# Kernel tuning notes

Hardware: AMD Instinct MI355X
Metric: run time of the kernel (lower is better)

Reference implementation:

```python
import jax, jax.numpy as jnp
import numpy as np

T = 524288
AABB = 4.0
BETA_MIN = 0.1
L_ENC = 4
NL = np.array([16, 22, 30, 42, 58, 80, 111, 154, 213, 295, 407, 563, 777, 1074, 1483, 2048])
# corner offsets, same ordering as the torch code's vertices[:,0..7]
OFFS = np.array([[0,0,0],[1,0,0],[0,1,0],[1,1,0],[0,0,1],[1,0,1],[0,1,1],[1,1,1]])
PRIMES = np.array([1, 2654435761, 805459861], dtype=np.uint32)


def hash_features(xn, tables):
    # xn: [N,3] normalized positions in hash-grid space; tables: [16, T, 2]
    Ns = jnp.asarray(NL, jnp.float32)                      # [16]
    xs = xn[:, None, :] * Ns[None, :, None]                # [N,16,3]
    fl = jnp.floor(xs)
    loc = xs - fl                                          # trilinear weights input
    fli = fl.astype(jnp.int32).astype(jnp.uint32)          # wraparound == int32 bit pattern
    offs = jnp.asarray(OFFS, jnp.uint32)                   # [8,3]
    pr = jnp.asarray(PRIMES, jnp.uint32)
    # spatial hash per corner, per level (avoid materializing [N,16,8,3] vertices)
    a = (fli[:, :, None, 0] + offs[None, None, :, 0]) * pr[0]
    b = (fli[:, :, None, 1] + offs[None, None, :, 1]) * pr[1]
    c = (fli[:, :, None, 2] + offs[None, None, :, 2]) * pr[2]
    h = ((a ^ b) ^ c) % jnp.uint32(T)                      # [N,16,8]
    lvl_off = (jnp.arange(len(NL), dtype=jnp.uint32) * jnp.uint32(T))[None, :, None]
    flat_idx = (h + lvl_off).astype(jnp.int32)             # index into flattened tables
    feats = tables.reshape(-1, tables.shape[-1])[flat_idx] # [N,16,8,2] gather
    offf = jnp.asarray(OFFS, jnp.float32)
    lp = loc[:, :, None, :]
    w = jnp.prod(lp * offf + (1.0 - lp) * (1.0 - offf), axis=-1)  # [N,16,8]
    out = jnp.einsum('nlc,nlcf->nlf', w, feats)            # trilinear interp
    return out.reshape(out.shape[0], -1)                   # [N, 16*2], level-major


def pos_enc(d):
    parts = [d]
    for j in range(L_ENC):
        parts.append(jnp.sin((2.0 ** j) * d))
        parts.append(jnp.cos((2.0 ** j) * d))
    return jnp.concatenate(parts, axis=1)                  # [N,27]


def _forward(x, d, appearance_idx, transient_idx, tables, emb_a, emb_t,
             Wd1, bd1, Wd2, bd2, Ws1, bs1, Ws2, bs2, Ws3, bs3,
             Wt1, bt1, Wt2, bt2, Wt3, bt3, Wtd, btd, Wtr, btr, Wtb, btb):
    xn = x / AABB
    mask = (jnp.abs(xn[:, 0]) < 0.5) & (jnp.abs(xn[:, 1]) < 0.5) & (jnp.abs(xn[:, 2]) < 0.5)
    xn = xn + 0.5
    feats = hash_features(xn, tables)                      # [N,32]
    h = jnp.maximum(feats @ Wd1 + bd1, 0.0) @ Wd2 + bd2    # density MLP -> [N,16]
    denc = pos_enc(d)
    a_emb = emb_a[appearance_idx]
    t_emb = emb_t[transient_idx]
    s = jnp.concatenate([h, denc, a_emb], axis=1)
    s = jnp.maximum(s @ Ws1 + bs1, 0.0)
    s = jnp.maximum(s @ Ws2 + bs2, 0.0)
    srgb = jax.nn.sigmoid(s @ Ws3 + bs3)
    t = jnp.concatenate([h, t_emb], axis=1)
    t = jnp.maximum(t @ Wt1 + bt1, 0.0)
    t = jnp.maximum(t @ Wt2 + bt2, 0.0)
    t = jnp.maximum(t @ Wt3 + bt3, 0.0)
    tsig = jax.nn.softplus(t @ Wtd + btd)[:, 0]
    trgb = jax.nn.sigmoid(t @ Wtr + btr)
    tbeta = jax.nn.softplus(t @ Wtb + btb)[:, 0] + BETA_MIN
    m = mask[:, None]
    static_rgb = jnp.where(m, srgb, 0.0)
    static_sigma = jnp.exp(jnp.where(mask, h[:, 0], -100000.0))
    transient_rgb = jnp.where(m, trgb, 0.0)
    transient_sigma = jnp.exp(jnp.where(mask, tsig, -100000.0))
    transient_beta = jnp.where(mask, tbeta, BETA_MIN)
    return static_rgb, static_sigma, transient_rgb, transient_sigma, transient_beta


def setup_inputs() -> dict:
    key = jax.random.key(0)
    ks = jax.random.split(key, 24)
    N, NV = 262144, 1000

    def lin(k, i, o):
        return jax.random.normal(k, (i, o), jnp.float32) * (1.0 / np.sqrt(i))

    inp = {}
    inp['x'] = jax.random.normal(ks[0], (N, 3), jnp.float32)
    inp['d'] = jax.random.normal(ks[1], (N, 3), jnp.float32)
    inp['appearance_idx'] = jax.random.randint(ks[2], (N,), 0, NV)
    inp['transient_idx'] = jax.random.randint(ks[3], (N,), 0, NV)
    inp['tables'] = (jax.random.uniform(ks[4], (len(NL), T, 2), jnp.float32) * 2 - 1) * 1e-4
    inp['emb_a'] = jax.random.normal(ks[5], (NV, 48), jnp.float32)
    inp['emb_t'] = jax.random.normal(ks[6], (NV, 16), jnp.float32)
    inp['Wd1'] = lin(ks[7], 32, 64); inp['bd1'] = jnp.zeros((64,), jnp.float32)
    inp['Wd2'] = lin(ks[8], 64, 16); inp['bd2'] = jnp.zeros((16,), jnp.float32)
    inp['Ws1'] = lin(ks[9], 91, 64); inp['bs1'] = jnp.zeros((64,), jnp.float32)
    inp['Ws2'] = lin(ks[10], 64, 64); inp['bs2'] = jnp.zeros((64,), jnp.float32)
    inp['Ws3'] = lin(ks[11], 64, 3); inp['bs3'] = jnp.zeros((3,), jnp.float32)
    inp['Wt1'] = lin(ks[12], 32, 64); inp['bt1'] = jnp.zeros((64,), jnp.float32)
    inp['Wt2'] = lin(ks[13], 64, 64); inp['bt2'] = jnp.zeros((64,), jnp.float32)
    inp['Wt3'] = lin(ks[14], 64, 64); inp['bt3'] = jnp.zeros((64,), jnp.float32)
    inp['Wtd'] = lin(ks[15], 64, 1); inp['btd'] = jnp.zeros((1,), jnp.float32)
    inp['Wtr'] = lin(ks[16], 64, 3); inp['btr'] = jnp.zeros((3,), jnp.float32)
    inp['Wtb'] = lin(ks[17], 64, 1); inp['btb'] = jnp.zeros((1,), jnp.float32)
    return inp


def reference(x, d, appearance_idx, transient_idx, tables, emb_a, emb_t,
              Wd1, bd1, Wd2, bd2, Ws1, bs1, Ws2, bs2, Ws3, bs3,
              Wt1, bt1, Wt2, bt2, Wt3, bt3, Wtd, btd, Wtr, btr, Wtb, btb):
    return _forward(x, d, appearance_idx, transient_idx, tables, emb_a, emb_t,
                    Wd1, bd1, Wd2, bd2, Ws1, bs1, Ws2, bs2, Ws3, bs3,
                    Wt1, bt1, Wt2, bt2, Wt3, bt3, Wtd, btd, Wtr, btr, Wtb, btb)
```

## Files before the change

kernel.cpp:

```cpp
#include <hip/hip_runtime.h>
#include <hip/hip_fp16.h>
#include <math.h>

#define NT 256
#define NT0 512
#define T_SIZE 524288u
#define T_MASK 524287u
#define PR1 2654435761u
#define PR2 805459861u

#define OFF_WD1 0
#define OFF_WD2 4096
#define OFF_WS1 6144
#define OFF_WS2 18432
#define OFF_WT1 26624
#define OFF_WT2 30720
#define OFF_WT3 38912
#define WBUF_USH 47104
#define WBUF_BYTES 98304

typedef float f32x4 __attribute__((ext_vector_type(4)));
typedef short s16x8 __attribute__((ext_vector_type(8)));
typedef unsigned u32x4 __attribute__((ext_vector_type(4)));

__device__ __forceinline__ float sigmoidf_(float x) { return 1.0f / (1.0f + __expf(-x)); }
__device__ __forceinline__ float softplusf_(float x) { return fmaxf(x, 0.0f) + log1pf(__expf(-fabsf(x))); }

__device__ __forceinline__ unsigned short f2bf(float f) {
  union { float f; unsigned u; } v; v.f = f;
  unsigned r = v.u + 0x7fffu + ((v.u >> 16) & 1u);
  return (unsigned short)(r >> 16);
}
__device__ __forceinline__ float bf2f(unsigned short h) {
  union { unsigned u; float f; } v; v.u = ((unsigned)h) << 16; return v.f;
}
__device__ __forceinline__ f32x4 splat4(float t) { f32x4 v; v[0]=t; v[1]=t; v[2]=t; v[3]=t; return v; }

__device__ __forceinline__ unsigned char f2e5(float f) {
  unsigned short u = __half_as_ushort(__float2half(f));
  return (unsigned char)(((unsigned)u + 0x7Fu + ((u >> 8) & 1u)) >> 8);
}
__device__ __forceinline__ float e52f(unsigned v) {
  return __half2float(__ushort_as_half((unsigned short)((v & 0xFFu) << 8)));
}

template <int ASTR, int SWM>
__device__ __forceinline__ s16x8 lda(const unsigned short* act, int lane, int m, int kh) {
  int p = m * 16 + (lane & 15);
  int c = (kh * 32 + ((lane >> 4) << 3)) ^ ((p & SWM) << 3);
  return *reinterpret_cast<const s16x8*>(act + p * ASTR + c);
}
__device__ __forceinline__ s16x8 ldb(const unsigned short* wb, int lane, int fidx) {
  return *reinterpret_cast<const s16x8*>(wb + (fidx * 64 + lane) * 8);
}
template <int ASTR, int SWM>
__device__ __forceinline__ void stp(unsigned short* act, int p, int col, float v0, float v1) {
  unsigned pk = (unsigned)f2bf(v0) | (((unsigned)f2bf(v1)) << 16);
  *reinterpret_cast<unsigned*>(act + p * ASTR + (col ^ ((p & SWM) << 3))) = pk;
}

template <int BT, int KH, int NTI, int NCOLS, class F>
__device__ void stage_plane(unsigned short* dst, const float* __restrict__ W, int plane, int tid, F rowmap) {
  for (int i = tid; i < NTI * KH * 64; i += BT) {
    int f = i >> 6, lane = i & 63;
    int n = f / KH, kh = f - n * KH;
    int o = n * 16 + (lane & 15);
    int kb = kh * 32 + ((lane >> 4) << 3);
    unsigned us0, us1, us2, us3;
#define MKPAIR(dstu, j0) { \
      unsigned short e0, e1; \
      { int sr = rowmap(kb + (j0)); float w = (sr >= 0) ? W[sr * NCOLS + o] : 0.f; \
        unsigned short hi = f2bf(w); e0 = plane ? f2bf(w - bf2f(hi)) : hi; } \
      { int sr = rowmap(kb + (j0) + 1); float w = (sr >= 0) ? W[sr * NCOLS + o] : 0.f; \
        unsigned short hi = f2bf(w); e1 = plane ? f2bf(w - bf2f(hi)) : hi; } \
      dstu = (unsigned)e0 | (((unsigned)e1) << 16); }
    MKPAIR(us0, 0) MKPAIR(us1, 2) MKPAIR(us2, 4) MKPAIR(us3, 6)
#undef MKPAIR
    *reinterpret_cast<uint4*>(dst + (size_t)i * 8) = make_uint4(us0, us1, us2, us3);
  }
}

template <int BT>
__device__ __forceinline__ void stage(float* dst, const float* __restrict__ src, int cnt, int tid) {
  for (int i = tid; i < cnt; i += BT) dst[i] = src[i];
}

template <int BT>
__device__ __forceinline__ void stagecpy(unsigned short* dst, const unsigned short* __restrict__ src,
                                         int cnt_ush, int tid) {
  const uint4* s = reinterpret_cast<const uint4*>(src);
  uint4* d = reinterpret_cast<uint4*>(dst);
  for (int i = tid; i < (cnt_ush >> 3); i += BT) d[i] = s[i];
}

#define MFMA_(a, b, c) __builtin_amdgcn_mfma_f32_16x16x32_bf16(a, b, c, 0, 0, 0)

#define DECL_ACC f32x4 acc00, acc01, acc02, acc03, acc10, acc11, acc12, acc13, \
                       acc20, acc21, acc22, acc23, acc30, acc31, acc32, acc33;

#define ACC_INIT(B) { \
  float t0 = (B)[(lane & 15)], t1 = (B)[16 + (lane & 15)], t2 = (B)[32 + (lane & 15)], t3 = (B)[48 + (lane & 15)]; \
  acc00 = splat4(t0); acc10 = acc00; acc20 = acc00; acc30 = acc00; \
  acc01 = splat4(t1); acc11 = acc01; acc21 = acc01; acc31 = acc01; \
  acc02 = splat4(t2); acc12 = acc02; acc22 = acc02; acc32 = acc02; \
  acc03 = splat4(t3); acc13 = acc03; acc23 = acc03; acc33 = acc03; }

#define GEMM_NBLK(WPTR, kh, KH, n) { s16x8 b = ldb(WPTR, lane, (n) * (KH) + (kh)); \
  acc0##n = MFMA_(a0, b, acc0##n); acc1##n = MFMA_(a1, b, acc1##n); \
  acc2##n = MFMA_(a2, b, acc2##n); acc3##n = MFMA_(a3, b, acc3##n); }

#define GEMM64(ACTP, ASTR, SWM, WB, KH, PLN) { \
  _Pragma("unroll") for (int kh = 0; kh < (KH); ++kh) { \
    s16x8 a0 = lda<ASTR, SWM>(ACTP, lane, 0, kh), a1 = lda<ASTR, SWM>(ACTP, lane, 1, kh), \
          a2 = lda<ASTR, SWM>(ACTP, lane, 2, kh), a3 = lda<ASTR, SWM>(ACTP, lane, 3, kh); \
    _Pragma("unroll") for (int pl = 0; pl < (PLN); ++pl) { \
      const unsigned short* wp = (WB) + pl * (KH) * 2048; \
      GEMM_NBLK(wp, kh, KH, 0) GEMM_NBLK(wp, kh, KH, 1) GEMM_NBLK(wp, kh, KH, 2) GEMM_NBLK(wp, kh, KH, 3) } } }

#define ST_ACT1(ACTP, ASTR, SWM, m, n, A) { \
  _Pragma("unroll") for (int r = 0; r < 4; ++r) { \
    int p = (m) * 16 + ((lane >> 4) << 2) + r; int col = (n) * 16 + (lane & 15); \
    (ACTP)[p * (ASTR) + (col ^ ((p & (SWM)) << 3))] = f2bf(fmaxf((A)[r], 0.f)); } }

#define ST_ACT_ALL(ACTP, ASTR, SWM) \
  ST_ACT1(ACTP, ASTR, SWM, 0, 0, acc00) ST_ACT1(ACTP, ASTR, SWM, 0, 1, acc01) \
  ST_ACT1(ACTP, ASTR, SWM, 0, 2, acc02) ST_ACT1(ACTP, ASTR, SWM, 0, 3, acc03) \
  ST_ACT1(ACTP, ASTR, SWM, 1, 0, acc10) ST_ACT1(ACTP, ASTR, SWM, 1, 1, acc11) \
  ST_ACT1(ACTP, ASTR, SWM, 1, 2, acc12) ST_ACT1(ACTP, ASTR, SWM, 1, 3, acc13) \
  ST_ACT1(ACTP, ASTR, SWM, 2, 0, acc20) ST_ACT1(ACTP, ASTR, SWM, 2, 1, acc21) \
  ST_ACT1(ACTP, ASTR, SWM, 2, 2, acc22) ST_ACT1(ACTP, ASTR, SWM, 2, 3, acc23) \
  ST_ACT1(ACTP, ASTR, SWM, 3, 0, acc30) ST_ACT1(ACTP, ASTR, SWM, 3, 1, acc31) \
  ST_ACT1(ACTP, ASTR, SWM, 3, 2, acc32) ST_ACT1(ACTP, ASTR, SWM, 3, 3, acc33)

#define ST_HV(ACTP, ASTR, SWM, m, H) { \
  _Pragma("unroll") for (int r = 0; r < 4; ++r) { \
    int pp = (m) * 16 + ((lane >> 4) << 2) + r; \
    (ACTP)[pp * (ASTR) + ((lane & 15) ^ ((pp & (SWM)) << 3))] = f2bf((H)[r]); } }

__global__ void __launch_bounds__(256) kwprep(
    const float* __restrict__ Wd1, const float* __restrict__ Wd2,
    const float* __restrict__ Ws1, const float* __restrict__ Ws2,
    const float* __restrict__ Wt1, const float* __restrict__ Wt2,
    const float* __restrict__ Wt3, unsigned short* __restrict__ wbuf) {
  const int pid = blockIdx.x, tid = threadIdx.x;
  const float* W;
  int KH, NTI, NCOLS, mapt, dst;
  switch (pid >> 1) {
    case 0: W = Wd1; KH = 1; NTI = 4; NCOLS = 64; mapt = 0; dst = OFF_WD1 + (pid & 1) * 2048; break;
    case 1: W = Wd2; KH = 2; NTI = 1; NCOLS = 16; mapt = 0; dst = OFF_WD2 + (pid & 1) * 1024; break;
    case 2: W = Ws1; KH = 3; NTI = 4; NCOLS = 64; mapt = 1; dst = OFF_WS1 + (pid & 1) * 6144; break;
    case 3: W = Ws2; KH = 2; NTI = 4; NCOLS = 64; mapt = 0; dst = OFF_WS2 + (pid & 1) * 4096; break;
    case 4: W = Wt1; KH = 1; NTI = 4; NCOLS = 64; mapt = 0; dst = OFF_WT1 + (pid & 1) * 2048; break;
    case 5: W = Wt2; KH = 2; NTI = 4; NCOLS = 64; mapt = 0; dst = OFF_WT2 + (pid & 1) * 4096; break;
    default: W = Wt3; KH = 2; NTI = 4; NCOLS = 64; mapt = 0; dst = OFF_WT3 + (pid & 1) * 4096; break;
  }
  const int plane = pid & 1;
  const int total = NTI * KH * 64;
  for (int i = tid; i < total; i += 256) {
    int f = i >> 6, lane = i & 63;
    int n = f / KH, kh = f - n * KH;
    int o = n * 16 + (lane & 15);
    int kb = kh * 32 + ((lane >> 4) << 3);
    unsigned short e[8];
#pragma unroll
    for (int j = 0; j < 8; ++j) {
      int k = kb + j;
      int sr = mapt ? (k < 16 ? k : (k < 64 ? 27 + k : (k < 91 ? k - 48 : -1))) : k;
      float w = (sr >= 0) ? W[sr * NCOLS + o] : 0.f;
      unsigned short hi = f2bf(w);
      e[j] = plane ? f2bf(w - bf2f(hi)) : hi;
    }
    uint4 v;
    v.x = (unsigned)e[0] | ((unsigned)e[1] << 16);
    v.y = (unsigned)e[2] | ((unsigned)e[3] << 16);
    v.z = (unsigned)e[4] | ((unsigned)e[5] << 16);
    v.w = (unsigned)e[6] | ((unsigned)e[7] << 16);
    *reinterpret_cast<uint4*>(wbuf + dst + (size_t)i * 8) = v;
  }
}

__global__ void __launch_bounds__(256) kconv(const float* __restrict__ tables,
                                             unsigned* __restrict__ t8, int nq) {
  int i = blockIdx.x * 256 + threadIdx.x;
  if (i >= nq) return;
  f32x4 v = __builtin_nontemporal_load(reinterpret_cast<const f32x4*>(tables) + i);
  unsigned r = (unsigned)f2e5(v[0]) | ((unsigned)f2e5(v[1]) << 8) |
               ((unsigned)f2e5(v[2]) << 16) | ((unsigned)f2e5(v[3]) << 24);
  __builtin_nontemporal_store(r, t8 + i);
}

__global__ void __launch_bounds__(256, 4) k0a_gather(
    const float* __restrict__ x, const unsigned short* __restrict__ t8,
    unsigned* __restrict__ featws, int Npts) {
  const int lane = threadIdx.x & 63, wv = threadIdx.x >> 6;
  const int g = blockIdx.x & 3;
  const int n = (blockIdx.x >> 2) * 256 + wv * 64 + lane;
  if (n >= Npts) return;
  float xn0 = x[3 * n + 0] * 0.25f + 0.5f;
  float xn1 = x[3 * n + 1] * 0.25f + 0.5f;
  float xn2 = x[3 * n + 2] * 0.25f + 0.5f;

  float scA, scB, scC, scD;
  switch (g) {
    case 0:  scA = 16.f; scB = 58.f;  scC = 213.f; scD = 777.f;  break;
    case 1:  scA = 22.f; scB = 80.f;  scC = 295.f; scD = 1074.f; break;
    case 2:  scA = 30.f; scB = 111.f; scC = 407.f; scD = 1483.f; break;
    default: scA = 42.f; scB = 154.f; scC = 563.f; scD = 2048.f; break;
  }

#define ALVL(J, SC) \
  unsigned ad##J##0, ad##J##1, ad##J##2, ad##J##3, ad##J##4, ad##J##5, ad##J##6, ad##J##7; \
  float lf##J##0, lf##J##1, lf##J##2; \
  { \
    float xs0 = xn0 * (SC), xs1 = xn1 * (SC), xs2 = xn2 * (SC); \
    float f0 = floorf(xs0), f1 = floorf(xs1), f2 = floorf(xs2); \
    lf##J##0 = xs0 - f0; lf##J##1 = xs1 - f1; lf##J##2 = xs2 - f2; \
    unsigned i0 = (unsigned)(int)f0, i1 = (unsigned)(int)f1, i2 = (unsigned)(int)f2; \
    unsigned a0 = i0, a1 = i0 + 1u; \
    unsigned b0 = i1 * PR1, b1 = (i1 + 1u) * PR1; \
    unsigned c0 = i2 * PR2, c1 = (i2 + 1u) * PR2; \
    unsigned base = (unsigned)(g + 4 * (J)) * T_SIZE; \
    ad##J##0 = (base + ((a0 ^ b0 ^ c0) & T_MASK)) * 2u; \
    ad##J##1 = (base + ((a1 ^ b0 ^ c0) & T_MASK)) * 2u; \
    ad##J##2 = (base + ((a0 ^ b1 ^ c0) & T_MASK)) * 2u; \
    ad##J##3 = (base + ((a1 ^ b1 ^ c0) & T_MASK)) * 2u; \
    ad##J##4 = (base + ((a0 ^ b0 ^ c1) & T_MASK)) * 2u; \
    ad##J##5 = (base + ((a1 ^ b0 ^ c1) & T_MASK)) * 2u; \
    ad##J##6 = (base + ((a0 ^ b1 ^ c1) & T_MASK)) * 2u; \
    ad##J##7 = (base + ((a1 ^ b1 ^ c1) & T_MASK)) * 2u; \
  }
  ALVL(0, scA) ALVL(1, scB) ALVL(2, scC) ALVL(3, scD)
#undef ALVL

#define GLD(Q, AD) asm volatile("global_load_ushort %0, %1, %2" : "=v"(Q) : "v"(AD), "s"(t8));
#define LLVL(J) \
  unsigned q##J##0, q##J##1, q##J##2, q##J##3, q##J##4, q##J##5, q##J##6, q##J##7; \
  GLD(q##J##0, ad##J##0) GLD(q##J##1, ad##J##1) GLD(q##J##2, ad##J##2) GLD(q##J##3, ad##J##3) \
  GLD(q##J##4, ad##J##4) GLD(q##J##5, ad##J##5) GLD(q##J##6, ad##J##6) GLD(q##J##7, ad##J##7)
  LLVL(0) LLVL(1) LLVL(2) LLVL(3)
#undef LLVL
#undef GLD
  asm volatile("s_waitcnt vmcnt(0)" ::: "memory");
  __builtin_amdgcn_sched_barrier(0);

#define BLVL(J, FP) { \
    float w1x = lf##J##0, w0x = 1.f - w1x; \
    float w1y = lf##J##1, w0y = 1.f - w1y; \
    float w1z = lf##J##2, w0z = 1.f - w1z; \
    float w000 = w0x * w0y * w0z, w100 = w1x * w0y * w0z; \
    float w010 = w0x * w1y * w0z, w110 = w1x * w1y * w0z; \
    float w001 = w0x * w0y * w1z, w101 = w1x * w0y * w1z; \
    float w011 = w0x * w1y * w1z, w111 = w1x * w1y * w1z; \
    float fa = w000 * e52f(q##J##0) + w100 * e52f(q##J##1) + w010 * e52f(q##J##2) + \
               w110 * e52f(q##J##3) + w001 * e52f(q##J##4) + w101 * e52f(q##J##5) + \
               w011 * e52f(q##J##6) + w111 * e52f(q##J##7); \
    float fb = w000 * e52f(q##J##0 >> 8) + w100 * e52f(q##J##1 >> 8) + w010 * e52f(q##J##2 >> 8) + \
               w110 * e52f(q##J##3 >> 8) + w001 * e52f(q##J##4 >> 8) + w101 * e52f(q##J##5 >> 8) + \
               w011 * e52f(q##J##6 >> 8) + w111 * e52f(q##J##7 >> 8); \
    FP = (unsigned)f2bf(fa) | (((unsigned)f2bf(fb)) << 16); }
  unsigned fp0, fp1, fp2, fp3;
  BLVL(0, fp0) BLVL(1, fp1) BLVL(2, fp2) BLVL(3, fp3)
#undef BLVL
  u32x4 o; o[0] = fp0; o[1] = fp1; o[2] = fp2; o[3] = fp3;
  __builtin_nontemporal_store(
      o, reinterpret_cast<u32x4*>(featws + ((size_t)g * Npts + n) * 4));
}

__global__ void __launch_bounds__(NT, 2) k12b_all(
    const float* __restrict__ x, const float* __restrict__ d,
    const int* __restrict__ aidx, const int* __restrict__ tridx,
    const float* __restrict__ emb_a, const float* __restrict__ emb_t,
    const unsigned* __restrict__ featws, const unsigned short* __restrict__ wbuf,
    const float* __restrict__ bd1, const float* __restrict__ bd2,
    const float* __restrict__ bs1, const float* __restrict__ bs2,
    const float* __restrict__ Ws3, const float* __restrict__ bs3,
    const float* __restrict__ bt1, const float* __restrict__ bt2,
    const float* __restrict__ bt3,
    const float* __restrict__ Wtd, const float* __restrict__ btd,
    const float* __restrict__ Wtr, const float* __restrict__ btr,
    const float* __restrict__ Wtb, const float* __restrict__ btb,
    float* __restrict__ out, int Npts) {
  __shared__ __align__(16) unsigned short sh[36864];
  __shared__ __align__(16) float fl[1240];
  const int tid = threadIdx.x, lane = tid & 63, wv = tid >> 6;
  const int n = blockIdx.x * NT + tid;
  const bool live = (n < Npts);
  const int nn = live ? n : Npts - 1;
  unsigned short* actw = sh + wv * 6144;
  unsigned short* wreg = sh + 24576;
  const int p = lane;

  float xn0 = x[3 * nn + 0] * 0.25f, xn1 = x[3 * nn + 1] * 0.25f, xn2 = x[3 * nn + 2] * 0.25f;
  const bool mask = (fabsf(xn0) < 0.5f) && (fabsf(xn1) < 0.5f) && (fabsf(xn2) < 0.5f);

  u32x4 q0 = __builtin_nontemporal_load(
      reinterpret_cast<const u32x4*>(featws + ((size_t)0 * Npts + nn) * 4));
  u32x4 q1 = __builtin_nontemporal_load(
      reinterpret_cast<const u32x4*>(featws + ((size_t)1 * Npts + nn) * 4));
  u32x4 q2 = __builtin_nontemporal_load(
      reinterpret_cast<const u32x4*>(featws + ((size_t)2 * Npts + nn) * 4));
  u32x4 q3 = __builtin_nontemporal_load(
      reinterpret_cast<const u32x4*>(featws + ((size_t)3 * Npts + nn) * 4));
  const float4* tp = reinterpret_cast<const float4*>(emb_t + (size_t)tridx[nn] * 16);
  float4 et0 = tp[0], et1 = tp[1], et2 = tp[2], et3 = tp[3];

  {
    float d0 = d[3 * nn + 0], d1 = d[3 * nn + 1], d2 = d[3 * nn + 2];
    float s10 = __sinf(d0), s11 = __sinf(d1), s12 = __sinf(d2);
    float c10 = __cosf(d0), c11 = __cosf(d1), c12 = __cosf(d2);
    float s20 = __sinf(2.f * d0), s21 = __sinf(2.f * d1), s22 = __sinf(2.f * d2);
    float c20 = __cosf(2.f * d0), c21 = __cosf(2.f * d1), c22 = __cosf(2.f * d2);
    float s40 = __sinf(4.f * d0), s41 = __sinf(4.f * d1), s42 = __sinf(4.f * d2);
    float c40 = __cosf(4.f * d0), c41 = __cosf(4.f * d1), c42 = __cosf(4.f * d2);
    float s80 = __sinf(8.f * d0), s81 = __sinf(8.f * d1), s82 = __sinf(8.f * d2);
    float c80 = __cosf(8.f * d0), c81 = __cosf(8.f * d1), c82 = __cosf(8.f * d2);
    stp<96, 3>(actw, p, 64, d0, d1);   stp<96, 3>(actw, p, 66, d2, s10);
    stp<96, 3>(actw, p, 68, s11, s12); stp<96, 3>(actw, p, 70, c10, c11);
    stp<96, 3>(actw, p, 72, c12, s20); stp<96, 3>(actw, p, 74, s21, s22);
    stp<96, 3>(actw, p, 76, c20, c21); stp<96, 3>(actw, p, 78, c22, s40);
    stp<96, 3>(actw, p, 80, s41, s42); stp<96, 3>(actw, p, 82, c40, c41);
    stp<96, 3>(actw, p, 84, c42, s80); stp<96, 3>(actw, p, 86, s81, s82);
    stp<96, 3>(actw, p, 88, c80, c81); stp<96, 3>(actw, p, 90, c82, 0.f);
    stp<96, 3>(actw, p, 92, 0.f, 0.f); stp<96, 3>(actw, p, 94, 0.f, 0.f);
  }
#define PUTL96(l, val) *reinterpret_cast<unsigned*>(actw + p * 96 + ((2 * (l)) ^ ((p & 3) << 3))) = (val);
  PUTL96(0, q0[0]) PUTL96(4, q0[1]) PUTL96(8, q0[2]) PUTL96(12, q0[3])
  PUTL96(1, q1[0]) PUTL96(5, q1[1]) PUTL96(9, q1[2]) PUTL96(13, q1[3])
  PUTL96(2, q2[0]) PUTL96(6, q2[1]) PUTL96(10, q2[2]) PUTL96(14, q2[3])
  PUTL96(3, q3[0]) PUTL96(7, q3[1]) PUTL96(11, q3[2]) PUTL96(15, q3[3])
#undef PUTL96

  stagecpy<NT>(wreg, wbuf + OFF_WD1, 4096, tid);
  stagecpy<NT>(wreg + 4096, wbuf + OFF_WD2, 2048, tid);
  stage<NT>(fl, bs1, 64, tid);
  stage<NT>(fl + 64, bs2, 64, tid);
  stage<NT>(fl + 128, Ws3, 192, tid);
  if (tid < 3) fl[320 + tid] = bs3[tid];
  stage<NT>(fl + 384, bt1, 64, tid);
  stage<NT>(fl + 448, bt2, 64, tid);
  stage<NT>(fl + 512, bt3, 64, tid);
  stage<NT>(fl + 576, Wtd, 64, tid);
  stage<NT>(fl + 640, Wtr, 192, tid);
  stage<NT>(fl + 832, Wtb, 64, tid);
  if (tid == 0) { fl[896] = btd[0]; fl[900] = btb[0]; }
  if (tid < 3) fl[897 + tid] = btr[tid];
  stage<NT>(fl + 904, bd1, 64, tid);
  stage<NT>(fl + 968, bd2, 16, tid);
  __syncthreads();

  DECL_ACC;
  ACC_INIT(fl + 904);
  GEMM64(actw, 96, 3, wreg, 1, 2);
  ST_ACT_ALL(actw, 96, 3);

  f32x4 h0, h1, h2, h3;
  { float t = fl[968 + (lane & 15)]; h0 = splat4(t); h1 = h0; h2 = h0; h3 = h0; }
#pragma unroll
  for (int kh = 0; kh < 2; ++kh) {
    s16x8 a0 = lda<96, 3>(actw, lane, 0, kh), a1 = lda<96, 3>(actw, lane, 1, kh),
          a2 = lda<96, 3>(actw, lane, 2, kh), a3 = lda<96, 3>(actw, lane, 3, kh);
#pragma unroll
    for (int pl = 0; pl < 2; ++pl) {
      s16x8 b = ldb(wreg + 4096 + pl * 1024, lane, kh);
      h0 = MFMA_(a0, b, h0); h1 = MFMA_(a1, b, h1); h2 = MFMA_(a2, b, h2); h3 = MFMA_(a3, b, h3);
    }
  }
#define HV_X(m, H) { _Pragma("unroll") for (int r = 0; r < 4; ++r) { \
    int pr = (m) * 16 + ((lane >> 4) << 2) + r; \
    if ((lane & 15) == 0) fl[984 + wv * 64 + pr] = (H)[r]; } }
  HV_X(0, h0) HV_X(1, h1) HV_X(2, h2) HV_X(3, h3)
#undef HV_X
  ST_HV(actw, 96, 3, 0, h0) ST_HV(actw, 96, 3, 1, h1)
  ST_HV(actw, 96, 3, 2, h2) ST_HV(actw, 96, 3, 3, h3)
  {
    float hv0v = fl[984 + wv * 64 + lane];
    if (live) out[3 * (size_t)Npts + n] = mask ? __expf(hv0v) : 0.f;
  }
  {
    const float4* ap = reinterpret_cast<const float4*>(emb_a + (size_t)aidx[nn] * 48);
#pragma unroll
    for (int q = 0; q < 12; ++q) {
      float4 e = ap[q];
      stp<96, 3>(actw, p, 16 + 4 * q, e.x, e.y);
      stp<96, 3>(actw, p, 18 + 4 * q, e.z, e.w);
    }
  }
  __syncthreads();
  stagecpy<NT>(wreg, wbuf + OFF_WS1, 12288, tid);
  __syncthreads();

  ACC_INIT(fl);
  GEMM64(actw, 96, 3, wreg, 3, 2);
  ST_ACT_ALL(actw, 96, 3);
  __syncthreads();
  stagecpy<NT>(wreg, wbuf + OFF_WS2, 8192, tid);
  __syncthreads();
  ACC_INIT(fl + 64);
  GEMM64(actw, 96, 3, wreg, 2, 2);
  ST_ACT_ALL(actw, 96, 3);

  {
    float r0 = fl[320], r1 = fl[321], r2 = fl[322];
    for (int j = 0; j < 64; ++j) {
      float a = bf2f(actw[p * 96 + (j ^ ((p & 3) << 3))]);
      r0 = fmaf(a, fl[128 + 3 * j + 0], r0);
      r1 = fmaf(a, fl[128 + 3 * j + 1], r1);
      r2 = fmaf(a, fl[128 + 3 * j + 2], r2);
    }
    if (live) {
      out[3 * (size_t)n + 0] = mask ? sigmoidf_(r0) : 0.f;
      out[3 * (size_t)n + 1] = mask ? sigmoidf_(r1) : 0.f;
      out[3 * (size_t)n + 2] = mask ? sigmoidf_(r2) : 0.f;
    }
  }

  ST_HV(actw, 96, 3, 0, h0) ST_HV(actw, 96, 3, 1, h1)
  ST_HV(actw, 96, 3, 2, h2) ST_HV(actw, 96, 3, 3, h3)
  stp<96, 3>(actw, p, 16, et0.x, et0.y);  stp<96, 3>(actw, p, 18, et0.z, et0.w);
  stp<96, 3>(actw, p, 20, et1.x, et1.y);  stp<96, 3>(actw, p, 22, et1.z, et1.w);
  stp<96, 3>(actw, p, 24, et2.x, et2.y);  stp<96, 3>(actw, p, 26, et2.z, et2.w);
  stp<96, 3>(actw, p, 28, et3.x, et3.y);  stp<96, 3>(actw, p, 30, et3.z, et3.w);
  __syncthreads();
  stagecpy<NT>(wreg, wbuf + OFF_WT1, 4096, tid);
  __syncthreads();
  ACC_INIT(fl + 384);
  GEMM64(actw, 96, 3, wreg, 1, 2);
  ST_ACT_ALL(actw, 96, 3);
  __syncthreads();
  stagecpy<NT>(wreg, wbuf + OFF_WT2, 8192, tid);
  __syncthreads();
  ACC_INIT(fl + 448);
  GEMM64(actw, 96, 3, wreg, 2, 2);
  ST_ACT_ALL(actw, 96, 3);
  __syncthreads();
  stagecpy<NT>(wreg, wbuf + OFF_WT3, 8192, tid);
  __syncthreads();
  ACC_INIT(fl + 512);
  GEMM64(actw, 96, 3, wreg, 2, 2);
  ST_ACT_ALL(actw, 96, 3);

  float hd = fl[896], hr0 = fl[897], hr1 = fl[898], hr2 = fl[899], hb = fl[900];
  for (int j = 0; j < 64; ++j) {
    float a = bf2f(actw[p * 96 + (j ^ ((p & 3) << 3))]);
    hd = fmaf(a, fl[576 + j], hd);
    hr0 = fmaf(a, fl[640 + 3 * j + 0], hr0);
    hr1 = fmaf(a, fl[640 + 3 * j + 1], hr1);
    hr2 = fmaf(a, fl[640 + 3 * j + 2], hr2);
    hb = fmaf(a, fl[832 + j], hb);
  }
  if (live) {
    size_t N4 = (size_t)Npts * 4;
    out[N4 + 3 * (size_t)n + 0] = mask ? sigmoidf_(hr0) : 0.f;
    out[N4 + 3 * (size_t)n + 1] = mask ? sigmoidf_(hr1) : 0.f;
    out[N4 + 3 * (size_t)n + 2] = mask ? sigmoidf_(hr2) : 0.f;
    out[(size_t)Npts * 7 + n] = mask ? __expf(softplusf_(hd)) : 0.f;
    out[(size_t)Npts * 8 + n] = mask ? (softplusf_(hb) + 0.1f) : 0.1f;
  }
}

template <int F8>
__global__ void __launch_bounds__(NT0, 4) k0f_density(
    const float* __restrict__ x, const float* __restrict__ tables,
    const unsigned short* __restrict__ t8,
    const float* __restrict__ Wd1, const float* __restrict__ bd1,
    const float* __restrict__ Wd2, const float* __restrict__ bd2,
    float* __restrict__ hvws, float* __restrict__ out, int Npts) {
  __shared__ __align__(16) unsigned short sh[38912];
  __shared__ __align__(16) float fl[592];
  const int tid = threadIdx.x, lane = tid & 63, wv = tid >> 6;
  const int n = blockIdx.x * NT0 + tid;
  const bool live = (n < Npts);
  const int nn = live ? n : Npts - 1;

  stage_plane<NT0, 1, 4, 64>(sh + 32768, Wd1, 0, tid, [](int k) { return k; });
  stage_plane<NT0, 1, 4, 64>(sh + 32768 + 2048, Wd1, 1, tid, [](int k) { return k; });
  stage_plane<NT0, 2, 1, 16>(sh + 36864, Wd2, 0, tid, [](int k) { return k; });
  stage_plane<NT0, 2, 1, 16>(sh + 36864 + 1024, Wd2, 1, tid, [](int k) { return k; });
  stage<NT0>(fl, bd1, 64, tid);
  stage<NT0>(fl + 64, bd2, 16, tid);
  __syncthreads();

  unsigned short* actw = sh + wv * 4096;
  const int p = lane;
  float xn0 = x[3 * nn + 0] * 0.25f + 0.5f, xn1 = x[3 * nn + 1] * 0.25f + 0.5f, xn2 = x[3 * nn + 2] * 0.25f + 0.5f;
  const bool mask = (fabsf(xn0 - 0.5f) < 0.5f) && (fabsf(xn1 - 0.5f) < 0.5f) && (fabsf(xn2 - 0.5f) < 0.5f);

  const float2* tab2 = reinterpret_cast<const float2*>(tables);
  constexpr float NLV[16] = {16.f, 22.f, 30.f, 42.f, 58.f, 80.f, 111.f, 154.f,
                             213.f, 295.f, 407.f, 563.f, 777.f, 1074.f, 1483.f, 2048.f};
#pragma unroll
  for (int l = 0; l < 16; ++l) {
    const float sc = NLV[l];
    float xs0 = xn0 * sc, xs1 = xn1 * sc, xs2 = xn2 * sc;
    float f0 = floorf(xs0), f1 = floorf(xs1), f2 = floorf(xs2);
    float l0 = xs0 - f0, l1 = xs1 - f1, l2 = xs2 - f2;
    unsigned i0 = (unsigned)(int)f0, i1 = (unsigned)(int)f1, i2 = (unsigned)(int)f2;
    unsigned a0 = i0, a1 = i0 + 1u;
    unsigned b0 = i1 * PR1, b1 = (i1 + 1u) * PR1;
    unsigned c0 = i2 * PR2, c1 = (i2 + 1u) * PR2;
    float w0x = 1.f - l0, w1x = l0, w0y = 1.f - l1, w1y = l1, w0z = 1.f - l2, w1z = l2;
    float2 t0, t1, t2, t3, t4, t5, t6, t7;
    if constexpr (F8) {
      const unsigned short* tl8 = t8 + (size_t)l * T_SIZE;
      unsigned short q0 = tl8[(a0 ^ b0 ^ c0) & T_MASK];
      unsigned short q1 = tl8[(a1 ^ b0 ^ c0) & T_MASK];
      unsigned short q2 = tl8[(a0 ^ b1 ^ c0) & T_MASK];
      unsigned short q3 = tl8[(a1 ^ b1 ^ c0) & T_MASK];
      unsigned short q4 = tl8[(a0 ^ b0 ^ c1) & T_MASK];
      unsigned short q5 = tl8[(a1 ^ b0 ^ c1) & T_MASK];
      unsigned short q6 = tl8[(a0 ^ b1 ^ c1) & T_MASK];
      unsigned short q7 = tl8[(a1 ^ b1 ^ c1) & T_MASK];
      t0 = make_float2(e52f(q0), e52f(q0 >> 8));
      t1 = make_float2(e52f(q1), e52f(q1 >> 8));
      t2 = make_float2(e52f(q2), e52f(q2 >> 8));
      t3 = make_float2(e52f(q3), e52f(q3 >> 8));
      t4 = make_float2(e52f(q4), e52f(q4 >> 8));
      t5 = make_float2(e52f(q5), e52f(q5 >> 8));
      t6 = make_float2(e52f(q6), e52f(q6 >> 8));
      t7 = make_float2(e52f(q7), e52f(q7 >> 8));
    } else {
      const float2* tl = tab2 + (size_t)l * T_SIZE;
      t0 = tl[(a0 ^ b0 ^ c0) & T_MASK];
      t1 = tl[(a1 ^ b0 ^ c0) & T_MASK];
      t2 = tl[(a0 ^ b1 ^ c0) & T_MASK];
      t3 = tl[(a1 ^ b1 ^ c0) & T_MASK];
      t4 = tl[(a0 ^ b0 ^ c1) & T_MASK];
      t5 = tl[(a1 ^ b0 ^ c1) & T_MASK];
      t6 = tl[(a0 ^ b1 ^ c1) & T_MASK];
      t7 = tl[(a1 ^ b1 ^ c1) & T_MASK];
    }
    float w000 = w0x * w0y * w0z, w100 = w1x * w0y * w0z;
    float w010 = w0x * w1y * w0z, w110 = w1x * w1y * w0z;
    float w001 = w0x * w0y * w1z, w101 = w1x * w0y * w1z;
    float w011 = w0x * w1y * w1z, w111 = w1x * w1y * w1z;
    float fa = w000 * t0.x + w100 * t1.x + w010 * t2.x + w110 * t3.x +
               w001 * t4.x + w101 * t5.x + w011 * t6.x + w111 * t7.x;
    float fb = w000 * t0.y + w100 * t1.y + w010 * t2.y + w110 * t3.y +
               w001 * t4.y + w101 * t5.y + w011 * t6.y + w111 * t7.y;
    unsigned pk = (unsigned)f2bf(fa) | (((unsigned)f2bf(fb)) << 16);
    *reinterpret_cast<unsigned*>(actw + p * 64 + ((2 * l) ^ ((p & 7) << 3))) = pk;
  }

  DECL_ACC;
  ACC_INIT(fl);
  GEMM64(actw, 64, 7, sh + 32768, 1, 2);
  ST_ACT_ALL(actw, 64, 7);

  f32x4 h0, h1, h2, h3;
  { float t = fl[64 + (lane & 15)]; h0 = splat4(t); h1 = h0; h2 = h0; h3 = h0; }
  {
#pragma unroll
    for (int kh = 0; kh < 2; ++kh) {
      s16x8 a0 = lda<64, 7>(actw, lane, 0, kh), a1 = lda<64, 7>(actw, lane, 1, kh),
            a2 = lda<64, 7>(actw, lane, 2, kh), a3 = lda<64, 7>(actw, lane, 3, kh);
#pragma unroll
      for (int pl = 0; pl < 2; ++pl) {
        s16x8 b = ldb(sh + 36864 + pl * 1024, lane, kh);
        h0 = MFMA_(a0, b, h0); h1 = MFMA_(a1, b, h1); h2 = MFMA_(a2, b, h2); h3 = MFMA_(a3, b, h3);
      }
    }
  }
  const int ptbase = blockIdx.x * NT0 + wv * 64;
#define HV_ST(m, H) { _Pragma("unroll") for (int r = 0; r < 4; ++r) { \
    int pr = (m) * 16 + ((lane >> 4) << 2) + r; \
    if (ptbase + pr < Npts) hvws[(size_t)(ptbase + pr) * 16 + (lane & 15)] = (H)[r]; \
    if ((lane & 15) == 0) fl[80 + wv * 64 + pr] = (H)[r]; } }
  HV_ST(0, h0) HV_ST(1, h1) HV_ST(2, h2) HV_ST(3, h3)
#undef HV_ST
  float hv0 = fl[80 + wv * 64 + lane];
  if (live) out[3 * (size_t)Npts + n] = mask ? __expf(hv0) : 0.f;
}

__global__ void __launch_bounds__(NT, 2) k12_heads(
    const float* __restrict__ x, const float* __restrict__ d,
    const int* __restrict__ aidx, const int* __restrict__ tridx,
    const float* __restrict__ emb_a, const float* __restrict__ emb_t,
    const unsigned short* __restrict__ wbuf,
    const float* __restrict__ bs1, const float* __restrict__ bs2,
    const float* __restrict__ Ws3, const float* __restrict__ bs3,
    const float* __restrict__ bt1, const float* __restrict__ bt2,
    const float* __restrict__ bt3,
    const float* __restrict__ Wtd, const float* __restrict__ btd,
    const float* __restrict__ Wtr, const float* __restrict__ btr,
    const float* __restrict__ Wtb, const float* __restrict__ btb,
    const float* __restrict__ hvws, float* __restrict__ out, int Npts) {
  __shared__ __align__(16) unsigned short sh[36864];
  __shared__ __align__(16) float fl[904];
  const int tid = threadIdx.x, lane = tid & 63, wv = tid >> 6;
  const int n = blockIdx.x * NT + tid;
  const bool live = (n < Npts);
  const int nn = live ? n : Npts - 1;
  unsigned short* actw = sh + wv * 6144;
  const int p = lane;

  float xn0 = x[3 * nn + 0] * 0.25f, xn1 = x[3 * nn + 1] * 0.25f, xn2 = x[3 * nn + 2] * 0.25f;
  const bool mask = (fabsf(xn0) < 0.5f) && (fabsf(xn1) < 0.5f) && (fabsf(xn2) < 0.5f);

  const float4* hvp = reinterpret_cast<const float4*>(hvws + (size_t)nn * 16);
  float4 hv0_ = hvp[0], hv1_ = hvp[1], hv2_ = hvp[2], hv3_ = hvp[3];
  const float4* tp = reinterpret_cast<const float4*>(emb_t + (size_t)tridx[nn] * 16);
  float4 et0 = tp[0], et1 = tp[1], et2 = tp[2], et3 = tp[3];

  {
    stp<96, 3>(actw, p, 0, hv0_.x, hv0_.y);   stp<96, 3>(actw, p, 2, hv0_.z, hv0_.w);
    stp<96, 3>(actw, p, 4, hv1_.x, hv1_.y);   stp<96, 3>(actw, p, 6, hv1_.z, hv1_.w);
    stp<96, 3>(actw, p, 8, hv2_.x, hv2_.y);   stp<96, 3>(actw, p, 10, hv2_.z, hv2_.w);
    stp<96, 3>(actw, p, 12, hv3_.x, hv3_.y);  stp<96, 3>(actw, p, 14, hv3_.z, hv3_.w);
    const float4* ap = reinterpret_cast<const float4*>(emb_a + (size_t)aidx[nn] * 48);
#pragma unroll
    for (int q = 0; q < 12; ++q) {
      float4 e = ap[q];
      stp<96, 3>(actw, p, 16 + 4 * q, e.x, e.y);
      stp<96, 3>(actw, p, 18 + 4 * q, e.z, e.w);
    }
    float d0 = d[3 * nn + 0], d1 = d[3 * nn + 1], d2 = d[3 * nn + 2];
    float s10 = __sinf(d0), s11 = __sinf(d1), s12 = __sinf(d2);
    float c10 = __cosf(d0), c11 = __cosf(d1), c12 = __cosf(d2);
    float s20 = __sinf(2.f * d0), s21 = __sinf(2.f * d1), s22 = __sinf(2.f * d2);
    float c20 = __cosf(2.f * d0), c21 = __cosf(2.f * d1), c22 = __cosf(2.f * d2);
    float s40 = __sinf(4.f * d0), s41 = __sinf(4.f * d1), s42 = __sinf(4.f * d2);
    float c40 = __cosf(4.f * d0), c41 = __cosf(4.f * d1), c42 = __cosf(4.f * d2);
    float s80 = __sinf(8.f * d0), s81 = __sinf(8.f * d1), s82 = __sinf(8.f * d2);
    float c80 = __cosf(8.f * d0), c81 = __cosf(8.f * d1), c82 = __cosf(8.f * d2);
    stp<96, 3>(actw, p, 64, d0, d1);   stp<96, 3>(actw, p, 66, d2, s10);
    stp<96, 3>(actw, p, 68, s11, s12); stp<96, 3>(actw, p, 70, c10, c11);
    stp<96, 3>(actw, p, 72, c12, s20); stp<96, 3>(actw, p, 74, s21, s22);
    stp<96, 3>(actw, p, 76, c20, c21); stp<96, 3>(actw, p, 78, c22, s40);
    stp<96, 3>(actw, p, 80, s41, s42); stp<96, 3>(actw, p, 82, c40, c41);
    stp<96, 3>(actw, p, 84, c42, s80); stp<96, 3>(actw, p, 86, s81, s82);
    stp<96, 3>(actw, p, 88, c80, c81); stp<96, 3>(actw, p, 90, c82, 0.f);
    stp<96, 3>(actw, p, 92, 0.f, 0.f); stp<96, 3>(actw, p, 94, 0.f, 0.f);
  }
  stagecpy<NT>(sh + 24576, wbuf + OFF_WS1, 12288, tid);
  stage<NT>(fl, bs1, 64, tid);
  stage<NT>(fl + 64, bs2, 64, tid);
  stage<NT>(fl + 128, Ws3, 192, tid);
  if (tid < 3) fl[320 + tid] = bs3[tid];
  stage<NT>(fl + 384, bt1, 64, tid);
  stage<NT>(fl + 448, bt2, 64, tid);
  stage<NT>(fl + 512, bt3, 64, tid);
  stage<NT>(fl + 576, Wtd, 64, tid);
  stage<NT>(fl + 640, Wtr, 192, tid);
  stage<NT>(fl + 832, Wtb, 64, tid);
  if (tid == 0) { fl[896] = btd[0]; fl[900] = btb[0]; }
  if (tid < 3) fl[897 + tid] = btr[tid];
  __syncthreads();

  DECL_ACC;
  ACC_INIT(fl);
  GEMM64(actw, 96, 3, sh + 24576, 3, 2);
  ST_ACT_ALL(actw, 96, 3);
  __syncthreads();
  stagecpy<NT>(sh + 24576, wbuf + OFF_WS2, 8192, tid);
  __syncthreads();
  ACC_INIT(fl + 64);
  GEMM64(actw, 96, 3, sh + 24576, 2, 2);
  ST_ACT_ALL(actw, 96, 3);

  {
    float r0 = fl[320], r1 = fl[321], r2 = fl[322];
    for (int j = 0; j < 64; ++j) {
      float a = bf2f(actw[p * 96 + (j ^ ((p & 3) << 3))]);
      r0 = fmaf(a, fl[128 + 3 * j + 0], r0);
      r1 = fmaf(a, fl[128 + 3 * j + 1], r1);
      r2 = fmaf(a, fl[128 + 3 * j + 2], r2);
    }
    if (live) {
      out[3 * (size_t)n + 0] = mask ? sigmoidf_(r0) : 0.f;
      out[3 * (size_t)n + 1] = mask ? sigmoidf_(r1) : 0.f;
      out[3 * (size_t)n + 2] = mask ? sigmoidf_(r2) : 0.f;
    }
  }

  stp<96, 3>(actw, p, 0, hv0_.x, hv0_.y);   stp<96, 3>(actw, p, 2, hv0_.z, hv0_.w);
  stp<96, 3>(actw, p, 4, hv1_.x, hv1_.y);   stp<96, 3>(actw, p, 6, hv1_.z, hv1_.w);
  stp<96, 3>(actw, p, 8, hv2_.x, hv2_.y);   stp<96, 3>(actw, p, 10, hv2_.z, hv2_.w);
  stp<96, 3>(actw, p, 12, hv3_.x, hv3_.y);  stp<96, 3>(actw, p, 14, hv3_.z, hv3_.w);
  stp<96, 3>(actw, p, 16, et0.x, et0.y);    stp<96, 3>(actw, p, 18, et0.z, et0.w);
  stp<96, 3>(actw, p, 20, et1.x, et1.y);    stp<96, 3>(actw, p, 22, et1.z, et1.w);
  stp<96, 3>(actw, p, 24, et2.x, et2.y);    stp<96, 3>(actw, p, 26, et2.z, et2.w);
  stp<96, 3>(actw, p, 28, et3.x, et3.y);    stp<96, 3>(actw, p, 30, et3.z, et3.w);
  __syncthreads();
  stagecpy<NT>(sh + 24576, wbuf + OFF_WT1, 4096, tid);
  __syncthreads();
  ACC_INIT(fl + 384);
  GEMM64(actw, 96, 3, sh + 24576, 1, 2);
  ST_ACT_ALL(actw, 96, 3);
  __syncthreads();
  stagecpy<NT>(sh + 24576, wbuf + OFF_WT2, 8192, tid);
  __syncthreads();
  ACC_INIT(fl + 448);
  GEMM64(actw, 96, 3, sh + 24576, 2, 2);
  ST_ACT_ALL(actw, 96, 3);
  __syncthreads();
  stagecpy<NT>(sh + 24576, wbuf + OFF_WT3, 8192, tid);
  __syncthreads();
  ACC_INIT(fl + 512);
  GEMM64(actw, 96, 3, sh + 24576, 2, 2);
  ST_ACT_ALL(actw, 96, 3);

  float hd = fl[896], hr0 = fl[897], hr1 = fl[898], hr2 = fl[899], hb = fl[900];
  for (int j = 0; j < 64; ++j) {
    float a = bf2f(actw[p * 96 + (j ^ ((p & 3) << 3))]);
    hd = fmaf(a, fl[576 + j], hd);
    hr0 = fmaf(a, fl[640 + 3 * j + 0], hr0);
    hr1 = fmaf(a, fl[640 + 3 * j + 1], hr1);
    hr2 = fmaf(a, fl[640 + 3 * j + 2], hr2);
    hb = fmaf(a, fl[832 + j], hb);
  }
  if (live) {
    size_t N4 = (size_t)Npts * 4;
    out[N4 + 3 * (size_t)n + 0] = mask ? sigmoidf_(hr0) : 0.f;
    out[N4 + 3 * (size_t)n + 1] = mask ? sigmoidf_(hr1) : 0.f;
    out[N4 + 3 * (size_t)n + 2] = mask ? sigmoidf_(hr2) : 0.f;
    out[(size_t)Npts * 7 + n] = mask ? __expf(softplusf_(hd)) : 0.f;
    out[(size_t)Npts * 8 + n] = mask ? (softplusf_(hb) + 0.1f) : 0.1f;
  }
}

extern "C" void kernel_launch(void* const* d_in, const int* in_sizes, int n_in,
                              void* d_out, int out_size, void* d_ws, size_t ws_size,
                              hipStream_t stream) {
  const int Npts = in_sizes[0] / 3;
  const float* x = (const float*)d_in[0];
  const float* d = (const float*)d_in[1];
  const int* aidx = (const int*)d_in[2];
  const int* tridx = (const int*)d_in[3];
  const float* tables = (const float*)d_in[4];
  const float* emb_a = (const float*)d_in[5];
  const float* emb_t = (const float*)d_in[6];
  const float* Wd1 = (const float*)d_in[7];
  const float* bd1 = (const float*)d_in[8];
  const float* Wd2 = (const float*)d_in[9];
  const float* bd2 = (const float*)d_in[10];
  const float* Ws1 = (const float*)d_in[11];
  const float* bs1 = (const float*)d_in[12];
  const float* Ws2 = (const float*)d_in[13];
  const float* bs2 = (const float*)d_in[14];
  const float* Ws3 = (const float*)d_in[15];
  const float* bs3 = (const float*)d_in[16];
  const float* Wt1 = (const float*)d_in[17];
  const float* bt1 = (const float*)d_in[18];
  const float* Wt2 = (const float*)d_in[19];
  const float* bt2 = (const float*)d_in[20];
  const float* Wt3 = (const float*)d_in[21];
  const float* bt3 = (const float*)d_in[22];
  const float* Wtd = (const float*)d_in[23];
  const float* btd = (const float*)d_in[24];
  const float* Wtr = (const float*)d_in[25];
  const float* btr = (const float*)d_in[26];
  const float* Wtb = (const float*)d_in[27];
// ... 44 lines not shown
```

Measured before the change: 173.2 us.

## Pad activation rows instead of XOR swizzle, stage gathers per level, merge WT1/WT2 staging

The per-wave activation buffer changes from a 96-element XOR-swizzled row to a 104-element padded row, so bank conflicts are avoided by padding rather than index swizzling. The scalar tail loops now rotate their start index per lane to spread LDS accesses across banks. In the hash-gather kernel, the single full vmcnt wait becomes staged waits so each level's interpolation can start once its loads arrive. The WT1 and WT2 weights are staged together, removing one barrier pair, and the exchange buffer moves into the weight region. The cost is more LDS use and a larger, more fragile shared-memory layout.

```diff
diff --git a/kernel.cpp b/kernel.cpp
--- a/kernel.cpp
+++ b/kernel.cpp
@@ -18,6 +18,8 @@
 #define OFF_WT3 38912
 #define WBUF_USH 47104
 #define WBUF_BYTES 98304
+
+#define AS 104
 
 typedef float f32x4 __attribute__((ext_vector_type(4)));
 typedef short s16x8 __attribute__((ext_vector_type(8)));
@@ -240,8 +242,6 @@
   LLVL(0) LLVL(1) LLVL(2) LLVL(3)
 #undef LLVL
 #undef GLD
-  asm volatile("s_waitcnt vmcnt(0)" ::: "memory");
-  __builtin_amdgcn_sched_barrier(0);
 
 #define BLVL(J, FP) { \
     float w1x = lf##J##0, w0x = 1.f - w1x; \
@@ -259,7 +259,18 @@
                w011 * e52f(q##J##6 >> 8) + w111 * e52f(q##J##7 >> 8); \
     FP = (unsigned)f2bf(fa) | (((unsigned)f2bf(fb)) << 16); }
   unsigned fp0, fp1, fp2, fp3;
-  BLVL(0, fp0) BLVL(1, fp1) BLVL(2, fp2) BLVL(3, fp3)
+  asm volatile("s_waitcnt vmcnt(24)" ::: "memory");
+  __builtin_amdgcn_sched_barrier(0);
+  BLVL(0, fp0)
+  asm volatile("s_waitcnt vmcnt(16)" ::: "memory");
+  __builtin_amdgcn_sched_barrier(0);
+  BLVL(1, fp1)
+  asm volatile("s_waitcnt vmcnt(8)" ::: "memory");
+  __builtin_amdgcn_sched_barrier(0);
+  BLVL(2, fp2)
+  asm volatile("s_waitcnt vmcnt(0)" ::: "memory");
+  __builtin_amdgcn_sched_barrier(0);
+  BLVL(3, fp3)
 #undef BLVL
   u32x4 o; o[0] = fp0; o[1] = fp1; o[2] = fp2; o[3] = fp3;
   __builtin_nontemporal_store(
@@ -280,14 +291,15 @@
     const float* __restrict__ Wtr, const float* __restrict__ btr,
     const float* __restrict__ Wtb, const float* __restrict__ btb,
     float* __restrict__ out, int Npts) {
-  __shared__ __align__(16) unsigned short sh[36864];
-  __shared__ __align__(16) float fl[1240];
+  __shared__ __align__(16) unsigned short sh[38912];
+  __shared__ __align__(16) float fl[984];
   const int tid = threadIdx.x, lane = tid & 63, wv = tid >> 6;
   const int n = blockIdx.x * NT + tid;
   const bool live = (n < Npts);
   const int nn = live ? n : Npts - 1;
-  unsigned short* actw = sh + wv * 6144;
-  unsigned short* wreg = sh + 24576;
+  unsigned short* actw = sh + wv * (64 * AS);
+  unsigned short* wreg = sh + 26624;
+  float* exch = reinterpret_cast<float*>(wreg + 6144);
   const int p = lane;
 
   float xn0 = x[3 * nn + 0] * 0.25f, xn1 = x[3 * nn + 1] * 0.25f, xn2 = x[3 * nn + 2] * 0.25f;
@@ -314,21 +326,21 @@
     float c40 = __cosf(4.f * d0), c41 = __cosf(4.f * d1), c42 = __cosf(4.f * d2);
     float s80 = __sinf(8.f * d0), s81 = __sinf(8.f * d1), s82 = __sinf(8.f * d2);
     float c80 = __cosf(8.f * d0), c81 = __cosf(8.f * d1), c82 = __cosf(8.f * d2);
-    stp<96, 3>(actw, p, 64, d0, d1);   stp<96, 3>(actw, p, 66, d2, s10);
-    stp<96, 3>(actw, p, 68, s11, s12); stp<96, 3>(actw, p, 70, c10, c11);
-    stp<96, 3>(actw, p, 72, c12, s20); stp<96, 3>(actw, p, 74, s21, s22);
-    stp<96, 3>(actw, p, 76, c20, c21); stp<96, 3>(actw, p, 78, c22, s40);
-    stp<96, 3>(actw, p, 80, s41, s42); stp<96, 3>(actw, p, 82, c40, c41);
-    stp<96, 3>(actw, p, 84, c42, s80); stp<96, 3>(actw, p, 86, s81, s82);
-    stp<96, 3>(actw, p, 88, c80, c81); stp<96, 3>(actw, p, 90, c82, 0.f);
-    stp<96, 3>(actw, p, 92, 0.f, 0.f); stp<96, 3>(actw, p, 94, 0.f, 0.f);
-  }
-#define PUTL96(l, val) *reinterpret_cast<unsigned*>(actw + p * 96 + ((2 * (l)) ^ ((p & 3) << 3))) = (val);
-  PUTL96(0, q0[0]) PUTL96(4, q0[1]) PUTL96(8, q0[2]) PUTL96(12, q0[3])
-  PUTL96(1, q1[0]) PUTL96(5, q1[1]) PUTL96(9, q1[2]) PUTL96(13, q1[3])
-  PUTL96(2, q2[0]) PUTL96(6, q2[1]) PUTL96(10, q2[2]) PUTL96(14, q2[3])
-  PUTL96(3, q3[0]) PUTL96(7, q3[1]) PUTL96(11, q3[2]) PUTL96(15, q3[3])
-#undef PUTL96
+    stp<AS, 0>(actw, p, 64, d0, d1);   stp<AS, 0>(actw, p, 66, d2, s10);
+    stp<AS, 0>(actw, p, 68, s11, s12); stp<AS, 0>(actw, p, 70, c10, c11);
+    stp<AS, 0>(actw, p, 72, c12, s20); stp<AS, 0>(actw, p, 74, s21, s22);
+    stp<AS, 0>(actw, p, 76, c20, c21); stp<AS, 0>(actw, p, 78, c22, s40);
+    stp<AS, 0>(actw, p, 80, s41, s42); stp<AS, 0>(actw, p, 82, c40, c41);
+    stp<AS, 0>(actw, p, 84, c42, s80); stp<AS, 0>(actw, p, 86, s81, s82);
+    stp<AS, 0>(actw, p, 88, c80, c81); stp<AS, 0>(actw, p, 90, c82, 0.f);
+    stp<AS, 0>(actw, p, 92, 0.f, 0.f); stp<AS, 0>(actw, p, 94, 0.f, 0.f);
+  }
+#define PUTL(l, val) *reinterpret_cast<unsigned*>(actw + p * AS + 2 * (l)) = (val);
+  PUTL(0, q0[0]) PUTL(4, q0[1]) PUTL(8, q0[2]) PUTL(12, q0[3])
+  PUTL(1, q1[0]) PUTL(5, q1[1]) PUTL(9, q1[2]) PUTL(13, q1[3])
+  PUTL(2, q2[0]) PUTL(6, q2[1]) PUTL(10, q2[2]) PUTL(14, q2[3])
+  PUTL(3, q3[0]) PUTL(7, q3[1]) PUTL(11, q3[2]) PUTL(15, q3[3])
+#undef PUTL
 
   stagecpy<NT>(wreg, wbuf + OFF_WD1, 4096, tid);
   stagecpy<NT>(wreg + 4096, wbuf + OFF_WD2, 2048, tid);
@@ -350,15 +362,15 @@
 
   DECL_ACC;
   ACC_INIT(fl + 904);
-  GEMM64(actw, 96, 3, wreg, 1, 2);
-  ST_ACT_ALL(actw, 96, 3);
+  GEMM64(actw, AS, 0, wreg, 1, 2);
+  ST_ACT_ALL(actw, AS, 0);
 
   f32x4 h0, h1, h2, h3;
   { float t = fl[968 + (lane & 15)]; h0 = splat4(t); h1 = h0; h2 = h0; h3 = h0; }
 #pragma unroll
   for (int kh = 0; kh < 2; ++kh) {
-    s16x8 a0 = lda<96, 3>(actw, lane, 0, kh), a1 = lda<96, 3>(actw, lane, 1, kh),
-          a2 = lda<96, 3>(actw, lane, 2, kh), a3 = lda<96, 3>(actw, lane, 3, kh);
+    s16x8 a0 = lda<AS, 0>(actw, lane, 0, kh), a1 = lda<AS, 0>(actw, lane, 1, kh),
+          a2 = lda<AS, 0>(actw, lane, 2, kh), a3 = lda<AS, 0>(actw, lane, 3, kh);
 #pragma unroll
     for (int pl = 0; pl < 2; ++pl) {
       s16x8 b = ldb(wreg + 4096 + pl * 1024, lane, kh);
@@ -367,13 +379,13 @@
   }
 #define HV_X(m, H) { _Pragma("unroll") for (int r = 0; r < 4; ++r) { \
     int pr = (m) * 16 + ((lane >> 4) << 2) + r; \
-    if ((lane & 15) == 0) fl[984 + wv * 64 + pr] = (H)[r]; } }
+    if ((lane & 15) == 0) exch[wv * 64 + pr] = (H)[r]; } }
   HV_X(0, h0) HV_X(1, h1) HV_X(2, h2) HV_X(3, h3)
 #undef HV_X
-  ST_HV(actw, 96, 3, 0, h0) ST_HV(actw, 96, 3, 1, h1)
-  ST_HV(actw, 96, 3, 2, h2) ST_HV(actw, 96, 3, 3, h3)
+  ST_HV(actw, AS, 0, 0, h0) ST_HV(actw, AS, 0, 1, h1)
+  ST_HV(actw, AS, 0, 2, h2) ST_HV(actw, AS, 0, 3, h3)
   {
-    float hv0v = fl[984 + wv * 64 + lane];
+    float hv0v = exch[wv * 64 + lane];
     if (live) out[3 * (size_t)Npts + n] = mask ? __expf(hv0v) : 0.f;
   }
   {
@@ -381,8 +393,8 @@
 #pragma unroll
     for (int q = 0; q < 12; ++q) {
       float4 e = ap[q];
-      stp<96, 3>(actw, p, 16 + 4 * q, e.x, e.y);
-      stp<96, 3>(actw, p, 18 + 4 * q, e.z, e.w);
+      stp<AS, 0>(actw, p, 16 + 4 * q, e.x, e.y);
+      stp<AS, 0>(actw, p, 18 + 4 * q, e.z, e.w);
     }
   }
   __syncthreads();
@@ -390,22 +402,23 @@
   __syncthreads();
 
   ACC_INIT(fl);
-  GEMM64(actw, 96, 3, wreg, 3, 2);
-  ST_ACT_ALL(actw, 96, 3);
+  GEMM64(actw, AS, 0, wreg, 3, 2);
+  ST_ACT_ALL(actw, AS, 0);
   __syncthreads();
   stagecpy<NT>(wreg, wbuf + OFF_WS2, 8192, tid);
   __syncthreads();
   ACC_INIT(fl + 64);
-  GEMM64(actw, 96, 3, wreg, 2, 2);
-  ST_ACT_ALL(actw, 96, 3);
+  GEMM64(actw, AS, 0, wreg, 2, 2);
+  ST_ACT_ALL(actw, AS, 0);
 
   {
     float r0 = fl[320], r1 = fl[321], r2 = fl[322];
     for (int j = 0; j < 64; ++j) {
-      float a = bf2f(actw[p * 96 + (j ^ ((p & 3) << 3))]);
-      r0 = fmaf(a, fl[128 + 3 * j + 0], r0);
-      r1 = fmaf(a, fl[128 + 3 * j + 1], r1);
-      r2 = fmaf(a, fl[128 + 3 * j + 2], r2);
+      int jj = (j + 2 * p) & 63;
+      float a = bf2f(actw[p * AS + jj]);
+      r0 = fmaf(a, fl[128 + 3 * jj + 0], r0);
+      r1 = fmaf(a, fl[128 + 3 * jj + 1], r1);
+      r2 = fmaf(a, fl[128 + 3 * jj + 2], r2);
     }
     if (live) {
       out[3 * (size_t)n + 0] = mask ? sigmoidf_(r0) : 0.f;
@@ -414,39 +427,38 @@
     }
   }
 
-  ST_HV(actw, 96, 3, 0, h0) ST_HV(actw, 96, 3, 1, h1)
-  ST_HV(actw, 96, 3, 2, h2) ST_HV(actw, 96, 3, 3, h3)
-  stp<96, 3>(actw, p, 16, et0.x, et0.y);  stp<96, 3>(actw, p, 18, et0.z, et0.w);
-  stp<96, 3>(actw, p, 20, et1.x, et1.y);  stp<96, 3>(actw, p, 22, et1.z, et1.w);
-  stp<96, 3>(actw, p, 24, et2.x, et2.y);  stp<96, 3>(actw, p, 26, et2.z, et2.w);
-  stp<96, 3>(actw, p, 28, et3.x, et3.y);  stp<96, 3>(actw, p, 30, et3.z, et3.w);
+  ST_HV(actw, AS, 0, 0, h0) ST_HV(actw, AS, 0, 1, h1)
+  ST_HV(actw, AS, 0, 2, h2) ST_HV(actw, AS, 0, 3, h3)
+  stp<AS, 0>(actw, p, 16, et0.x, et0.y);  stp<AS, 0>(actw, p, 18, et0.z, et0.w);
+  stp<AS, 0>(actw, p, 20, et1.x, et1.y);  stp<AS, 0>(actw, p, 22, et1.z, et1.w);
+  stp<AS, 0>(actw, p, 24, et2.x, et2.y);  stp<AS, 0>(actw, p, 26, et2.z, et2.w);
+  stp<AS, 0>(actw, p, 28, et3.x, et3.y);  stp<AS, 0>(actw, p, 30, et3.z, et3.w);
   __syncthreads();
   stagecpy<NT>(wreg, wbuf + OFF_WT1, 4096, tid);
+  stagecpy<NT>(wreg + 4096, wbuf + OFF_WT2, 8192, tid);
   __syncthreads();
   ACC_INIT(fl + 384);
-  GEMM64(actw, 96, 3, wreg, 1, 2);
-  ST_ACT_ALL(actw, 96, 3);
-  __syncthreads();
-  stagecpy<NT>(wreg, wbuf + OFF_WT2, 8192, tid);
-  __syncthreads();
+  GEMM64(actw, AS, 0, wreg, 1, 2);
+  ST_ACT_ALL(actw, AS, 0);
   ACC_INIT(fl + 448);
-  GEMM64(actw, 96, 3, wreg, 2, 2);
-  ST_ACT_ALL(actw, 96, 3);
+  GEMM64(actw, AS, 0, (wreg + 4096), 2, 2);
+  ST_ACT_ALL(actw, AS, 0);
   __syncthreads();
   stagecpy<NT>(wreg, wbuf + OFF_WT3, 8192, tid);
   __syncthreads();
   ACC_INIT(fl + 512);
-  GEMM64(actw, 96, 3, wreg, 2, 2);
-  ST_ACT_ALL(actw, 96, 3);
+  GEMM64(actw, AS, 0, wreg, 2, 2);
+  ST_ACT_ALL(actw, AS, 0);
 
   float hd = fl[896], hr0 = fl[897], hr1 = fl[898], hr2 = fl[899], hb = fl[900];
   for (int j = 0; j < 64; ++j) {
-    float a = bf2f(actw[p * 96 + (j ^ ((p & 3) << 3))]);
-    hd = fmaf(a, fl[576 + j], hd);
-    hr0 = fmaf(a, fl[640 + 3 * j + 0], hr0);
-    hr1 = fmaf(a, fl[640 + 3 * j + 1], hr1);
-    hr2 = fmaf(a, fl[640 + 3 * j + 2], hr2);
-    hb = fmaf(a, fl[832 + j], hb);
+    int jj = (j + 2 * p) & 63;
+    float a = bf2f(actw[p * AS + jj]);
+    hd = fmaf(a, fl[576 + jj], hd);
+    hr0 = fmaf(a, fl[640 + 3 * jj + 0], hr0);
+    hr1 = fmaf(a, fl[640 + 3 * jj + 1], hr1);
+    hr2 = fmaf(a, fl[640 + 3 * jj + 2], hr2);
+    hb = fmaf(a, fl[832 + jj], hb);
   }
   if (live) {
     size_t N4 = (size_t)Npts * 4;
```

Result: no change. 169.9 us (-1.9%).
